# Kernel optimization log

Hardware: AMD Instinct MI355X
Metric: run time of the kernel (lower is better)

## Reference

```python
import jax, jax.numpy as jnp
import numpy as np

EPS = 1e-07


def setup_inputs() -> dict:
    key = jax.random.key(0)
    k1, k2, k3 = jax.random.split(key, 3)
    B, T, R, F = 16, 512, 128, 32
    timesteps = jax.random.uniform(k1, (B, T, F), dtype=jnp.float32)          # observation times, > 0
    values = jax.random.normal(k2, (B, T, F), dtype=jnp.float32)              # observed values
    reference_timesteps = jax.random.uniform(k3, (B, R), dtype=jnp.float32)  # query times
    alpha = jnp.ones((1,), dtype=jnp.float32) * 50.0                          # learned bandwidth param (init a=50)
    return {"timesteps": timesteps, "values": values,
            "reference_timesteps": reference_timesteps, "alpha": alpha}


def reference(timesteps, values, reference_timesteps, alpha):
    # timesteps, values: [B, T, F]; reference_timesteps: [B, R]; alpha: [1]
    R = reference_timesteps.shape[1]
    t = timesteps[:, None, :, :]                       # [B, 1, T, F]
    r = reference_timesteps[:, :, None, None]          # [B, R, 1, 1]
    mask = (t > 0).astype(timesteps.dtype)             # [B, 1, T, F]
    # squared-exponential kernel with mask, normalized by R (as in intensity)
    dist = jnp.exp(-alpha[0] * (r - t) ** 2) * mask + EPS  # [B, R, T, F]
    dist = dist / R
    lam = dist.sum(axis=2)                             # [B, R, F]
    smooth = jnp.sum(dist * values[:, None, :, :], axis=2) / lam  # [B, R, F]
    return smooth
```

## Files before the change

kernel.cpp:

```cpp
#include <hip/hip_runtime.h>


constexpr int B_ = 16, T_ = 512, R_ = 128, F_ = 32;
constexpr int RB_ = 4;
constexpr int TC_ = 128;
constexpr int NC_ = T_ / TC_;
constexpr float EPS_ = 1e-7f;
constexpr float LOG2E_ = 1.4426950408889634f;

__global__ __launch_bounds__(256, 2) void ga_fused(
    const float* __restrict__ ts_g, const float* __restrict__ v_g,
    const float* __restrict__ ref_g, const float* __restrict__ alpha_g,
    float* __restrict__ out)
{
    __shared__ float2 tile[TC_ * F_];
    __shared__ float4 red[RB_ * F_];

    const int tid = threadIdx.x;
    const int f   = tid & 31;
    const int rl  = (tid >> 5) & (RB_ - 1);
    const int th  = tid >> 7;
    const int rb  = blockIdx.x % (R_ / RB_);
    const int b   = blockIdx.x / (R_ / RB_);
    const int r_idx = rb * RB_ + rl;

    const float r = ref_g[b * R_ + r_idx];
    const float c = -alpha_g[0] * LOG2E_;

    const float4* tsg4 = (const float4*)(ts_g + (size_t)b * T_ * F_);
    const float4* vg4  = (const float4*)(v_g  + (size_t)b * T_ * F_);

    float num = 0.f, den = 0.f, sv = 0.f;

    for (int ch = 0; ch < NC_; ++ch) {
        if (ch) __syncthreads();
        const int base4 = ch * (TC_ * F_ / 4);
        #pragma unroll
        for (int i = tid; i < TC_ * F_ / 4; i += 256) {
            float4 a = tsg4[base4 + i];
            float4 w = vg4[base4 + i];
            a.x = (a.x > 0.f) ? a.x : 2e19f;
            a.y = (a.y > 0.f) ? a.y : 2e19f;
            a.z = (a.z > 0.f) ? a.z : 2e19f;
            a.w = (a.w > 0.f) ? a.w : 2e19f;
            float4* dst = (float4*)tile + 2 * i;
            dst[0] = make_float4(a.x, w.x, a.y, w.y);
            dst[1] = make_float4(a.z, w.z, a.w, w.w);
        }
        __syncthreads();

        const float2* tp = tile + th * (TC_ / 2) * F_ + f;
        #pragma unroll 16
        for (int t = 0; t < TC_ / 2; ++t) {
            float2 a = tp[t * F_];
            float d = r - a.x;
            float e = __builtin_amdgcn_exp2f(c * d * d);
            num = fmaf(e, a.y, num);
            den += e;
            sv  += a.y;
        }
    }

    __syncthreads();
    if (th == 1) red[rl * F_ + f] = make_float4(num, den, sv, 0.f);
    __syncthreads();
    if (th == 0) {
        float4 o = red[rl * F_ + f];
        float n = (num + o.x) + EPS_ * (sv + o.z);
        float d = (den + o.y) + (float)T_ * EPS_;
        out[(b * R_ + r_idx) * F_ + f] = n / d;
    }
}

extern "C" void kernel_launch(void* const* d_in, const int* in_sizes, int n_in,
                              void* d_out, int out_size, void* d_ws, size_t ws_size,
                              hipStream_t stream) {
    const float* timesteps = (const float*)d_in[0];
    const float* values    = (const float*)d_in[1];
    const float* ref_ts    = (const float*)d_in[2];
    const float* alpha     = (const float*)d_in[3];
    float* out = (float*)d_out;

    ga_fused<<<B_ * (R_ / RB_), 256, 0, stream>>>(
        timesteps, values, ref_ts, alpha, out);
}
```

Baseline: 71.50 us.

## Split time chunk across four thread groups and use packed float2 math

Doubles the block size to 512 threads, so each chunk's 128 timesteps are split across four thread groups of 32 steps each instead of two groups of 64. The reduction grows to three partial slots in shared memory. The inner loop processes two timesteps at once with two-wide vector types, so the compiler can emit packed FP32 ops (v_pk_fma/mul/add) for the distance, multiply and accumulate. The aim is more parallel work per block and fewer ALU instructions, at the cost of higher register and occupancy pressure from launch_bounds(512,4).

```diff
diff --git a/kernel.cpp b/kernel.cpp
--- a/kernel.cpp
+++ b/kernel.cpp
@@ -8,13 +8,15 @@
 constexpr float EPS_ = 1e-7f;
 constexpr float LOG2E_ = 1.4426950408889634f;
 
-__global__ __launch_bounds__(256, 2) void ga_fused(
+typedef float v2f __attribute__((ext_vector_type(2)));
+
+__global__ __launch_bounds__(512, 4) void ga_fused(
     const float* __restrict__ ts_g, const float* __restrict__ v_g,
     const float* __restrict__ ref_g, const float* __restrict__ alpha_g,
     float* __restrict__ out)
 {
     __shared__ float2 tile[TC_ * F_];
-    __shared__ float4 red[RB_ * F_];
+    __shared__ float4 red[3][RB_ * F_];
 
     const int tid = threadIdx.x;
     const int f   = tid & 31;
@@ -26,17 +28,19 @@
 
     const float r = ref_g[b * R_ + r_idx];
     const float c = -alpha_g[0] * LOG2E_;
+    const v2f rr = {r, r};
+    const v2f cc = {c, c};
 
     const float4* tsg4 = (const float4*)(ts_g + (size_t)b * T_ * F_);
     const float4* vg4  = (const float4*)(v_g  + (size_t)b * T_ * F_);
 
-    float num = 0.f, den = 0.f, sv = 0.f;
+    v2f num = {0.f, 0.f}, den = {0.f, 0.f}, sv = {0.f, 0.f};
 
     for (int ch = 0; ch < NC_; ++ch) {
         if (ch) __syncthreads();
         const int base4 = ch * (TC_ * F_ / 4);
         #pragma unroll
-        for (int i = tid; i < TC_ * F_ / 4; i += 256) {
+        for (int i = tid; i < TC_ * F_ / 4; i += 512) {
             float4 a = tsg4[base4 + i];
             float4 w = vg4[base4 + i];
             a.x = (a.x > 0.f) ? a.x : 2e19f;
@@ -49,25 +53,35 @@
         }
         __syncthreads();
 
-        const float2* tp = tile + th * (TC_ / 2) * F_ + f;
-        #pragma unroll 16
-        for (int t = 0; t < TC_ / 2; ++t) {
-            float2 a = tp[t * F_];
-            float d = r - a.x;
-            float e = __builtin_amdgcn_exp2f(c * d * d);
-            num = fmaf(e, a.y, num);
+        const float2* tp = tile + (th * 32) * F_ + f;
+        #pragma unroll 8
+        for (int j = 0; j < 16; ++j) {
+            float2 a0 = tp[j * F_];
+            float2 a1 = tp[(j + 16) * F_];
+            v2f ts2 = {a0.x, a1.x};
+            v2f vv  = {a0.y, a1.y};
+            v2f d = rr - ts2;
+            v2f p = (cc * d) * d;
+            v2f e;
+            e.x = __builtin_amdgcn_exp2f(p.x);
+            e.y = __builtin_amdgcn_exp2f(p.y);
+            num += e * vv;
             den += e;
-            sv  += a.y;
+            sv  += vv;
         }
     }
 
-    __syncthreads();
-    if (th == 1) red[rl * F_ + f] = make_float4(num, den, sv, 0.f);
+    float fn = num.x + num.y, fd = den.x + den.y, fs = sv.x + sv.y;
+    if (th) red[th - 1][rl * F_ + f] = make_float4(fn, fd, fs, 0.f);
     __syncthreads();
     if (th == 0) {
-        float4 o = red[rl * F_ + f];
-        float n = (num + o.x) + EPS_ * (sv + o.z);
-        float d = (den + o.y) + (float)T_ * EPS_;
+        #pragma unroll
+        for (int k = 0; k < 3; ++k) {
+            float4 o = red[k][rl * F_ + f];
+            fn += o.x; fd += o.y; fs += o.z;
+        }
+        float n = fn + EPS_ * fs;
+        float d = fd + (float)T_ * EPS_;
         out[(b * R_ + r_idx) * F_ + f] = n / d;
     }
 }
@@ -81,6 +95,6 @@
     const float* alpha     = (const float*)d_in[3];
     float* out = (float*)d_out;
 
-    ga_fused<<<B_ * (R_ / RB_), 256, 0, stream>>>(
+    ga_fused<<<B_ * (R_ / RB_), 512, 0, stream>>>(
         timesteps, values, ref_ts, alpha, out);
 }
```

Result: faster. 70.04 us (-2.0%).
